# Optimization experiments

Hardware: AMD Instinct MI355X
Metric: run time of the kernel (lower is better)

The kernel has to match this reference:

```python
import jax, jax.numpy as jnp
import numpy as np

B, T, HID = 2, 2048, 1024
NH = 8
QK_DIM = 1024
V_DIM = 2048
SCALE_BASE = 512.0
GN_EPS = 1e-5


def _xpos_rotate(x, downscale):
    # x: [B, T, QK_DIM]; XPOS rotary embedding (syncdoth/RetNet, offset=0)
    d = QK_DIM
    dh = d // 2
    pos = jnp.arange(T, dtype=jnp.float32)
    # per-pair magnitude scale
    base_scale = (jnp.arange(0, d, 2, dtype=jnp.float32) + 0.4 * d) / (1.4 * d)  # [dh]
    scale = base_scale[None, :] ** (pos[:, None] / SCALE_BASE)  # [T, dh]
    if downscale:
        scale = 1.0 / scale
    inv_freq = 1.0 / (10000.0 ** (jnp.arange(dh, dtype=jnp.float32) / dh))
    sinusoid = pos[:, None] * inv_freq[None, :]  # [T, dh]
    sin = jnp.sin(sinusoid) * scale
    cos = jnp.cos(sinusoid) * scale
    # duplicate_interleave -> [T, d]
    sin = jnp.repeat(sin, 2, axis=-1)
    cos = jnp.repeat(cos, 2, axis=-1)
    x1 = x[..., 0::2]
    x2 = x[..., 1::2]
    rot = jnp.stack((-x2, x1), axis=-1).reshape(x.shape)  # rotate_every_two
    return x * cos[None] + rot * sin[None]


def setup_inputs() -> dict:
    key = jax.random.key(0)
    k1, k2, k3, k4 = jax.random.split(key, 4)
    x = jax.random.normal(k1, (B, T, HID), dtype=jnp.float32)
    Wqkv = jax.random.normal(k2, (HID, 2 * QK_DIM + V_DIM), dtype=jnp.float32) / np.sqrt(HID)
    Wg = jax.random.normal(k3, (HID, V_DIM), dtype=jnp.float32) / np.sqrt(HID)
    Wp = jax.random.normal(k4, (V_DIM, HID), dtype=jnp.float32) / np.sqrt(V_DIM)
    bp = jnp.zeros((HID,), dtype=jnp.float32)
    return {"x": x, "Wqkv": Wqkv, "Wg": Wg, "Wp": Wp, "bp": bp}


def reference(x, Wqkv, Wg, Wp, bp):
    # multi-scale decay (non-default gamma path)
    gamma = 1.0 - jnp.exp(jnp.linspace(np.log(1.0 / 32), np.log(1.0 / 512), NH)).astype(jnp.float32)  # [NH]

    qkv = x @ Wqkv  # [B,T,2qk+v]
    q, k, v = jnp.split(qkv, [QK_DIM, 2 * QK_DIM], axis=-1)
    q = _xpos_rotate(q, downscale=False)
    k = _xpos_rotate(k, downscale=True)

    dqk = QK_DIM // NH
    dv = V_DIM // NH
    q = q.reshape(B, T, NH, dqk).transpose(0, 2, 1, 3)  # [B,H,T,dqk]
    k = k.reshape(B, T, NH, dqk).transpose(0, 2, 1, 3)
    v = v.reshape(B, T, NH, dv).transpose(0, 2, 1, 3)   # [B,H,T,dv]

    # parallel decay mask: gamma^(i-j) for i>=j else 0  -> [H,T,T]
    idx = jnp.arange(T)
    expo = idx[:, None] - idx[None, :]
    expo_safe = jnp.where(expo >= 0, expo, 0).astype(jnp.float32)
    decay_mask = jnp.where(expo[None] >= 0, gamma[:, None, None] ** expo_safe[None], 0.0)  # [H,T,T]

    scores = jnp.einsum('bhid,bhjd->bhij', q, k) * (dqk ** -0.5)
    retention = jnp.einsum('bhij,bhjv->bhiv', scores * decay_mask[None], v)  # [B,H,T,dv]

    # current_kv state: sum_t decay_mask[h,-1,t] * k_t (outer) v_t  -> [B,H,dqk,dv]
    curr_kv = jnp.einsum('bhtk,bhtv,ht->bhkv', k, v, decay_mask[:, -1, :])

    ret = retention.transpose(0, 2, 1, 3).reshape(B, T, V_DIM)

    # GroupNorm(num_groups=NH, affine=False) over [B*T, V_DIM]
    g = ret.reshape(B, T, NH, dv)
    mu = jnp.mean(g, axis=-1, keepdims=True)
    var = jnp.var(g, axis=-1, keepdims=True)
    normed = ((g - mu) / jnp.sqrt(var + GN_EPS)).reshape(B, T, V_DIM)

    gate = jax.nn.silu(x @ Wg)
    out = (gate * normed) @ Wp + bp
    return out, curr_kv
```

## Files before the change

### kernel.cpp

```cpp
#include <hip/hip_runtime.h>

typedef unsigned short u16;
typedef unsigned int   u32;
typedef unsigned long long u64;

typedef __attribute__((ext_vector_type(8))) short bf8_t;
typedef __attribute__((ext_vector_type(4))) float f4_t;

#define DEVI __device__ __forceinline__
#define MFMA16(a,b,c) __builtin_amdgcn_mfma_f32_16x16x32_bf16((a),(b),(c),0,0,0)

#define BB   2
#define TT   2048
#define HIDN 1024
#define L0f  (-3.4657359027997265f)
#define DLf  (-0.3960841031714215f)
#define SCL  (0.08838834764831845f)

DEVI u16 f2b(float f) {
    u32 u = __float_as_uint(f);
    u += 0x7FFFu + ((u >> 16) & 1u);
    return (u16)(u >> 16);
}
DEVI float b2f(u16 u) { return __uint_as_float(((u32)u) << 16); }

DEVI void gll16(const void* g, void* l) {
    __builtin_amdgcn_global_load_lds((const __attribute__((address_space(1))) void*)g,
                                     (__attribute__((address_space(3))) void*)l, 16, 0, 0);
}

__global__ __launch_bounds__(256) void k_prep(
    const float* __restrict__ x, const float* __restrict__ Wqkv,
    const float* __restrict__ Wg, const float* __restrict__ Wp,
    u32* __restrict__ cqp, u32* __restrict__ ckp,
    float* __restrict__ gt, float* __restrict__ gk,
    u16* __restrict__ xb, u16* __restrict__ oQ, u16* __restrict__ oG, u16* __restrict__ oP) {
    int bx = blockIdx.x;
    if (bx < 4096) {
        int idx = bx * 256 + threadIdx.x;
        int t = idx >> 9, m = idx & 511;
        float base = (2.f * (float)m + 409.6f) * (1.f / 1433.6f);
        float s = exp2f(log2f(base) * ((float)t * (1.f / 512.f)));
        float invf = exp2f(-(float)m * (13.287712379549449f / 512.f));
        float sn, cs;
        sincosf((float)t * invf, &sn, &cs);
        int h = m >> 6;
        float lg2h = log2f(1.f - expf(L0f + (float)h * DLf));
        float qf = s * SCL * exp2f((float)(t & 63) * lg2h);
        cqp[idx] = (u32)f2b(cs * qf) | ((u32)f2b(sn * qf) << 16);
        float is = 1.f / s;
        ckp[idx] = (u32)f2b(cs * is) | ((u32)f2b(sn * is) << 16);
        return;
    }
    if (bx < 4162) {
        int i = (bx - 4096) * 256 + threadIdx.x;
        if (i < 16384) {
            int h = i >> 11, t = i & 2047;
            float lg2 = log2f(1.f - expf(L0f + (float)h * DLf));
            gt[i] = exp2f((float)(2047 - t) * lg2);
        } else {
            int idx = i - 16384;
            int h = idx >> 6, d = idx & 63;
            float lg2 = log2f(1.f - expf(L0f + (float)h * DLf));
            gk[idx] = exp2f(-(float)d * lg2);
        }
        return;
    }
    if (bx < 12354) {
        __shared__ float tile[32][33];
        int b2 = bx - 4162;
        const float* in; u16* out; int R, C, cx, ry;
        if (b2 < 4096)      { in = Wqkv; out = oQ; R = 1024; C = 4096; cx = b2 & 127; ry = b2 >> 7; }
        else if (b2 < 6144) { int b3 = b2 - 4096; in = Wg; out = oG; R = 1024; C = 2048; cx = b3 & 63; ry = b3 >> 6; }
        else                { int b3 = b2 - 6144; in = Wp; out = oP; R = 2048; C = 1024; cx = b3 & 31; ry = b3 >> 5; }
        int c0 = cx * 32, r0 = ry * 32;
        int tx = threadIdx.x & 31, ty = threadIdx.x >> 5;
#pragma unroll
        for (int i = 0; i < 4; i++)
            tile[ty * 4 + i][tx] = in[(size_t)(r0 + ty * 4 + i) * C + c0 + tx];
        __syncthreads();
#pragma unroll
        for (int i = 0; i < 4; i++)
            out[(size_t)(c0 + ty * 4 + i) * R + r0 + tx] = f2b(tile[tx][ty * 4 + i]);
        return;
    }
    {
        int i = (bx - 12354) * 256 + threadIdx.x;
        float4 v = ((const float4*)x)[i];
        u64 pk = (u64)f2b(v.x) | ((u64)f2b(v.y) << 16) | ((u64)f2b(v.z) << 32) | ((u64)f2b(v.w) << 48);
        ((u64*)xb)[i] = pk;
    }
}

DEVI void stage_chunk(const u16* __restrict__ A, const u16* __restrict__ B,
                      int m0, int n0, int kt, char* buf, int id, int wid, int lane) {
    int j = id & 3;
    int flat = j * 8192 + wid * 1024 + lane * 16;
    int row = flat >> 7, byt = (flat & 127) ^ ((row & 7) << 4);
    if (id < 4)
        gll16((const char*)A + (size_t)(m0 + row) * 2048 + kt * 128 + byt,
              buf + j * 8192 + wid * 1024);
    else
        gll16((const char*)B + (size_t)(n0 + row) * 2048 + kt * 128 + byt,
              buf + 32768 + j * 8192 + wid * 1024);
}

#define QCORE(kk, fmh, LOADB)                                                         \
    {                                                                                 \
        bf8_t a_[4];                                                                  \
        _Pragma("unroll")                                                             \
        for (int f = 0; f < 4; f++) {                                                 \
            int ra = 128 * wr + ((fmh) * 4 + f) * 16 + lr;                            \
            a_[f] = *(const bf8_t*)(bA + ra * 128 + (((kk) * 64 + lg * 16) ^ ((ra & 7) << 4))); \
        }                                                                             \
        if (LOADB) {                                                                  \
            _Pragma("unroll")                                                         \
            for (int f = 0; f < 4; f++) {                                             \
                int rb = 64 * wc + f * 16 + lr;                                       \
                breg[f] = *(const bf8_t*)(bB + rb * 128 + (((kk) * 64 + lg * 16) ^ ((rb & 7) << 4))); \
            }                                                                         \
        }                                                                             \
        __builtin_amdgcn_s_barrier();                                                 \
        __builtin_amdgcn_s_setprio(1);                                                \
        _Pragma("unroll")                                                             \
        for (int f = 0; f < 4; f++)                                                   \
            _Pragma("unroll")                                                         \
            for (int j = 0; j < 4; j++)                                               \
                acc[(fmh) * 4 + f][j] = MFMA16(a_[f], breg[j], acc[(fmh) * 4 + f][j]); \
        __builtin_amdgcn_s_setprio(0);                                                \
    }

__global__ __launch_bounds__(512, 2) void k_gemm_qkvg8(
    const u16* __restrict__ xb, const u16* __restrict__ Wcat,
    const u32* __restrict__ cqp, const u32* __restrict__ ckp, const float* __restrict__ gkt,
    u16* __restrict__ qw, u16* __restrict__ kw, u16* __restrict__ kT, u16* __restrict__ vT,
    u16* __restrict__ gateb) {
    __shared__ __align__(16) char L[131072];
    int flat = blockIdx.x;
    int swz = (flat & 7) * 48 + (flat >> 3);
    int m0 = (swz / 24) * 256, n0 = (swz % 24) * 256;
    int tid = threadIdx.x, lane = tid & 63, wid = tid >> 6;
    int wr = wid >> 2, wc = wid & 3, lr = lane & 15, lg = lane >> 4;
    f4_t acc[8][4];
#pragma unroll
    for (int i = 0; i < 8; i++)
#pragma unroll
        for (int j = 0; j < 4; j++)
#pragma unroll
            for (int e = 0; e < 4; e++) acc[i][j][e] = 0.f;
    stage_chunk(xb, Wcat, m0, n0, 0, L, 0, wid, lane);
    stage_chunk(xb, Wcat, m0, n0, 0, L, 2, wid, lane);
    stage_chunk(xb, Wcat, m0, n0, 0, L, 4, wid, lane);
    stage_chunk(xb, Wcat, m0, n0, 0, L, 5, wid, lane);
    stage_chunk(xb, Wcat, m0, n0, 0, L, 6, wid, lane);
    stage_chunk(xb, Wcat, m0, n0, 0, L, 7, wid, lane);
    stage_chunk(xb, Wcat, m0, n0, 0, L, 1, wid, lane);
    stage_chunk(xb, Wcat, m0, n0, 0, L, 3, wid, lane);
    asm volatile("s_waitcnt vmcnt(2)" ::: "memory");
    __builtin_amdgcn_s_barrier();
    for (int kt = 0; kt < 16; ++kt) {
        const char* bA = L + (kt & 1) * 65536;
        const char* bB = bA + 32768;
        char* nbuf = L + ((kt + 1) & 1) * 65536;
        bf8_t breg[4];
        if (kt < 15) {
            stage_chunk(xb, Wcat, m0, n0, kt + 1, nbuf, 0, wid, lane);
            stage_chunk(xb, Wcat, m0, n0, kt + 1, nbuf, 2, wid, lane);
        }
        QCORE(0, 0, 1)
        if (kt < 15) { asm volatile("s_waitcnt vmcnt(2)" ::: "memory"); }
        else         { asm volatile("s_waitcnt vmcnt(0)" ::: "memory"); }
        __builtin_amdgcn_s_barrier();
        if (kt < 15) {
            stage_chunk(xb, Wcat, m0, n0, kt + 1, nbuf, 4, wid, lane);
            stage_chunk(xb, Wcat, m0, n0, kt + 1, nbuf, 5, wid, lane);
        }
        QCORE(0, 1, 0)
        __builtin_amdgcn_s_barrier();
        if (kt < 15) {
            stage_chunk(xb, Wcat, m0, n0, kt + 1, nbuf, 6, wid, lane);
            stage_chunk(xb, Wcat, m0, n0, kt + 1, nbuf, 7, wid, lane);
        }
        QCORE(1, 0, 1)
        __builtin_amdgcn_s_barrier();
        if (kt < 15) {
            stage_chunk(xb, Wcat, m0, n0, kt + 1, nbuf, 1, wid, lane);
            stage_chunk(xb, Wcat, m0, n0, kt + 1, nbuf, 3, wid, lane);
        }
        QCORE(1, 1, 0)
        if (kt < 15) { asm volatile("s_waitcnt vmcnt(2)" ::: "memory"); }
        __builtin_amdgcn_s_barrier();
    }
    __syncthreads();
    char* SP = L;
    int b = m0 >> 11, t0 = m0 & 2047;
    if (n0 < 4096 && n0 >= 2048) {
        int h = (n0 - 2048) >> 8;
#pragma unroll
        for (int fm = 0; fm < 8; fm++)
#pragma unroll
            for (int fn = 0; fn < 4; fn++) {
                int dv = wc * 64 + fn * 16 + lr;
                int rowb = wr * 128 + fm * 16 + lg * 4;
                u64 pk = 0;
#pragma unroll
                for (int r = 0; r < 4; r++) pk |= ((u64)f2b(acc[fm][fn][r])) << (16 * r);
                *(u64*)(SP + dv * 512 + ((rowb * 2) ^ ((dv & 15) << 4))) = pk;
            }
        __syncthreads();
#pragma unroll
        for (int it = 0; it < 16; it++) {
            int chunk = it * 512 + tid;
            int dv = chunk >> 5, j = chunk & 31;
            uint4 v = *(const uint4*)(SP + dv * 512 + ((j * 16) ^ ((dv & 15) << 4)));
            *(uint4*)(vT + ((size_t)((b * 8 + h) * 256 + dv)) * 2048 + t0 + j * 8) = v;
        }
    } else if (n0 < 2048) {
        int isK = n0 >= 1024;
        const u32* cT = isK ? ckp : cqp;
        int hb = (n0 >> 7) & 7;
#pragma unroll
        for (int fm = 0; fm < 8; fm++)
#pragma unroll
            for (int fn = 0; fn < 4; fn++) {
                int col = wc * 64 + fn * 16 + lr;
                int gq = (n0 & 1023) + col;
                int mi = gq >> 1, h = gq >> 7;
                u64 pk = 0;
#pragma unroll
                for (int r = 0; r < 4; r++) {
                    int rowl = wr * 128 + fm * 16 + lg * 4 + r;
                    int t = t0 + rowl;
                    float v = acc[fm][fn][r];
                    float pv = __shfl_xor(v, 1);
                    u32 cp = cT[t * 512 + mi];
                    float cs = b2f((u16)cp), sn = b2f((u16)(cp >> 16));
                    float o = (col & 1) ? (v * cs + pv * sn) : (v * cs - pv * sn);
                    if (isK) {
                        pk |= ((u64)f2b(o)) << (16 * r);
                        o *= gkt[h * 64 + (t & 63)];
                    }
                    *(u16*)(SP + rowl * 512 + ((col * 2) ^ ((rowl & 15) << 4))) = f2b(o);
                }
                if (isK)
                    *(u64*)&kT[((size_t)((b * 8 + h) * 128 + (gq & 127))) * 2048 + t0 + wr * 128 + fm * 16 + lg * 4] = pk;
            }
        __syncthreads();
#pragma unroll
        for (int it = 0; it < 16; it++) {
            int chunk = it * 512 + tid;
            int r = chunk >> 5, j = chunk & 31;
            uint4 v = *(const uint4*)(SP + r * 512 + ((j * 16) ^ ((r & 15) << 4)));
            int hh = hb + (j >> 4);
            u16* g = (isK ? kw : qw) + ((size_t)((b * 8 + hh) * 2048 + t0 + r)) * 128 + (j & 15) * 8;
            *(uint4*)g = v;
        }
    } else {
        int c0 = n0 - 4096;
#pragma unroll
        for (int fm = 0; fm < 8; fm++)
#pragma unroll
            for (int fn = 0; fn < 4; fn++) {
                int col = wc * 64 + fn * 16 + lr;
#pragma unroll
                for (int r = 0; r < 4; r++) {
                    int rowl = wr * 128 + fm * 16 + lg * 4 + r;
                    float gg = acc[fm][fn][r];
                    *(u16*)(SP + rowl * 512 + ((col * 2) ^ ((rowl & 15) << 4))) = f2b(gg / (1.f + expf(-gg)));
                }
            }
        __syncthreads();
#pragma unroll
        for (int it = 0; it < 16; it++) {
            int chunk = it * 512 + tid;
            int r = chunk >> 5, j = chunk & 31;
            uint4 v = *(const uint4*)(SP + r * 512 + ((j * 16) ^ ((r & 15) << 4)));
            *(uint4*)(gateb + (size_t)(b * 2048 + t0 + r) * 2048 + c0 + j * 8) = v;
        }
    }
}

DEVI void stage_o(const u16* __restrict__ A, const u16* __restrict__ B,
                  int m0, int n0, int kt, char* buf, int id, int wid, int lane) {
    int j = id & 1;
    int flat = j * 8192 + wid * 1024 + lane * 16;
    int row = flat >> 7, byt = (flat & 127) ^ ((row & 7) << 4);
    if (id < 2)
        gll16((const char*)A + (size_t)(m0 + row) * 4096 + kt * 128 + byt,
              buf + j * 8192 + wid * 1024);
    else
        gll16((const char*)B + (size_t)(n0 + row) * 4096 + kt * 128 + byt,
              buf + 16384 + j * 8192 + wid * 1024);
}

__global__ __launch_bounds__(512, 2) void k_gemm_out2(const u16* __restrict__ gdb,
                                                      const u16* __restrict__ Wt,
                                                      const float* __restrict__ bp,
                                                      float* __restrict__ outp) {
    __shared__ __align__(16) char Lo[98304];
    int m0 = blockIdx.y * 128, n0 = blockIdx.x * 128;
    int tid = threadIdx.x, lane = tid & 63, wid = tid >> 6;
    int wr = wid >> 1, wc = wid & 1, lr = lane & 15, lg = lane >> 4;
    f4_t acc[2][4];
#pragma unroll
    for (int i = 0; i < 2; i++)
#pragma unroll
        for (int j = 0; j < 4; j++)
#pragma unroll
            for (int e = 0; e < 4; e++) acc[i][j][e] = 0.f;
#pragma unroll
    for (int c = 0; c < 4; c++) stage_o(gdb, Wt, m0, n0, 0, Lo, c, wid, lane);
#pragma unroll
    for (int c = 0; c < 4; c++) stage_o(gdb, Wt, m0, n0, 1, Lo + 32768, c, wid, lane);
    asm volatile("s_waitcnt vmcnt(4)" ::: "memory");
    __builtin_amdgcn_s_barrier();
    for (int kt = 0; kt < 32; ++kt) {
        const char* bA = Lo + (kt % 3) * 32768;
        const char* bB = bA + 16384;
        if (kt < 30) {
            char* nbuf = Lo + ((kt + 2) % 3) * 32768;
#pragma unroll
            for (int c = 0; c < 4; c++) stage_o(gdb, Wt, m0, n0, kt + 2, nbuf, c, wid, lane);
        }
        __builtin_amdgcn_s_setprio(1);
#pragma unroll
        for (int kk = 0; kk < 2; kk++) {
            bf8_t a[2], b[4];
#pragma unroll
            for (int f = 0; f < 2; f++) {
                int ra = wr * 32 + f * 16 + lr;
                a[f] = *(const bf8_t*)(bA + ra * 128 + ((kk * 64 + lg * 16) ^ ((ra & 7) << 4)));
            }
#pragma unroll
            for (int f = 0; f < 4; f++) {
                int rb = wc * 64 + f * 16 + lr;
                b[f] = *(const bf8_t*)(bB + rb * 128 + ((kk * 64 + lg * 16) ^ ((rb & 7) << 4)));
            }
#pragma unroll
            for (int i = 0; i < 2; i++)
#pragma unroll
                for (int j = 0; j < 4; j++)
                    acc[i][j] = MFMA16(a[i], b[j], acc[i][j]);
        }
        __builtin_amdgcn_s_setprio(0);
        if (kt < 30) { asm volatile("s_waitcnt vmcnt(4)" ::: "memory"); }
        else         { asm volatile("s_waitcnt vmcnt(0)" ::: "memory"); }
        __builtin_amdgcn_s_barrier();
    }
    __syncthreads();
    float* SMf = (float*)Lo;
    float bv[4];
#pragma unroll
    for (int fn = 0; fn < 4; fn++) bv[fn] = bp[n0 + wc * 64 + fn * 16 + lr];
#pragma unroll
    for (int fm = 0; fm < 2; fm++)
#pragma unroll
        for (int fn = 0; fn < 4; fn++) {
            int col = wc * 64 + fn * 16 + lr;
#pragma unroll
            for (int r = 0; r < 4; r++) {
                int rowl = wr * 32 + fm * 16 + lg * 4 + r;
                *(float*)((char*)SMf + rowl * 512 + ((col * 4) ^ ((rowl & 7) << 6))) = acc[fm][fn][r] + bv[fn];
            }
        }
    __syncthreads();
#pragma unroll
    for (int it2 = 0; it2 < 8; it2++) {
        int chunk = it2 * 512 + tid;
        int rowl = chunk >> 5, j = chunk & 31;
        f4_t v = *(const f4_t*)((const char*)SMf + rowl * 512 + ((j * 16) ^ ((rowl & 7) << 6)));
        *(f4_t*)((char*)outp + ((size_t)(m0 + rowl) * 1024 + n0) * 4 + j * 16) = v;
    }
}

DEVI void acc_zero(f4_t acc[4][4]) {
#pragma unroll
    for (int i = 0; i < 4; i++)
#pragma unroll
        for (int j = 0; j < 4; j++)
#pragma unroll
            for (int e = 0; e < 4; e++) acc[i][j][e] = 0.f;
}

__global__ __launch_bounds__(256, 3) void k_retention(const u16* __restrict__ qws, const u16* __restrict__ kws,
                                                      const u16* __restrict__ vTws,
                                                      u16* __restrict__ ret0, u16* __restrict__ ret1) {
    __shared__ u16 SMr[64 * 128 + 256 * 64];
    u16* Ks = SMr;
    u16* Vs = SMr + 64 * 128;
    int x = blockIdx.x;
    int it, jlo, jhi, toret1;
    if (x < 16)      { it = 15 - x;  jlo = 0;              jhi = it + 1;         toret1 = 0; }
    else if (x < 32) { it = x;       jlo = 0;              jhi = (it + 2) >> 1;  toret1 = 0; }
    else             { it = x - 16;  jlo = (it + 2) >> 1;  jhi = it + 1;         toret1 = 1; }
    int h = blockIdx.y, b = blockIdx.z;
    int bh = b * 8 + h;
    float lg2 = log2f(1.f - expf(L0f + (float)h * DLf));
    int i0 = it * 64;
    const u16* qbase = qws + (size_t)bh * 2048 * 128;
    const u16* kbase = kws + (size_t)bh * 2048 * 128;
    const u16* vbase = vTws + (size_t)bh * 256 * 2048;
    int tid = threadIdx.x, lane = tid & 63, w = tid >> 6, lr = lane & 15, lg = lane >> 4;
    bf8_t aq[4];
#pragma unroll
    for (int kk = 0; kk < 4; kk++)
        aq[kk] = *(const bf8_t*)((const char*)qbase + (size_t)(i0 + w * 16 + lr) * 256 + kk * 64 + lg * 16);
    f4_t racc[16];
#pragma unroll
    for (int f = 0; f < 16; f++)
#pragma unroll
        for (int e = 0; e < 4; e++) racc[f][e] = 0.f;
    for (int jt = jlo; jt < jhi; jt++) {
        int j0 = jt * 64;
        int diag = (jt == it);
        float tf = exp2f(64.f * (float)(it - jt) * lg2);
        __syncthreads();
#pragma unroll
        for (int p = 0; p < 4; p++) {
            int flat = p * 4096 + tid * 16;
            int row = flat >> 8, byt = (flat & 255) ^ ((row & 7) << 4);
            gll16((const char*)kbase + (size_t)(j0 + row) * 256 + byt, (char*)Ks + p * 4096 + w * 1024);
        }
#pragma unroll
        for (int p = 0; p < 8; p++) {
            int flat = p * 4096 + tid * 16;
            int row = flat >> 7, byt = (flat & 127) ^ ((row & 7) << 4);
            gll16((const char*)vbase + (size_t)row * 4096 + (size_t)j0 * 2 + byt,
                  (char*)Vs + p * 4096 + w * 1024);
        }
        __syncthreads();
        f4_t sacc[4];
#pragma unroll
        for (int f = 0; f < 4; f++)
#pragma unroll
            for (int e = 0; e < 4; e++) sacc[f][e] = 0.f;
#pragma unroll
        for (int kk = 0; kk < 4; kk++)
#pragma unroll
            for (int fn = 0; fn < 4; fn++) {
                int rb = fn * 16 + lr;
                bf8_t bb = *(const bf8_t*)((const char*)Ks + rb * 256 + ((kk * 64 + lg * 16) ^ ((rb & 7) << 4)));
                sacc[fn] = MFMA16(aq[kk], bb, sacc[fn]);
            }
        __syncthreads();
#pragma unroll
        for (int fn = 0; fn < 4; fn++)
#pragma unroll
            for (int r = 0; r < 4; r++) {
                int i_loc = w * 16 + lg * 4 + r;
                int col = fn * 16 + lr;
                float v = diag ? ((i_loc - col >= 0) ? sacc[fn][r] : 0.f) : sacc[fn][r] * tf;
                *(u16*)((char*)Ks + i_loc * 128 + ((col * 2) ^ ((i_loc & 7) << 4))) = f2b(v);
            }
#pragma unroll
        for (int kk = 0; kk < 2; kk++) {
            int ra = w * 16 + lr;
            bf8_t ap = *(const bf8_t*)((const char*)Ks + ra * 128 + ((kk * 64 + lg * 16) ^ ((ra & 7) << 4)));
#pragma unroll
            for (int fn2 = 0; fn2 < 16; fn2++) {
                int rb = fn2 * 16 + lr;
                bf8_t bv = *(const bf8_t*)((const char*)Vs + rb * 128 + ((kk * 64 + lg * 16) ^ ((rb & 7) << 4)));
                racc[fn2] = MFMA16(ap, bv, racc[fn2]);
            }
        }
    }
    __syncthreads();
    u16* St = Vs;
#pragma unroll
    for (int fn2 = 0; fn2 < 16; fn2++)
#pragma unroll
        for (int r = 0; r < 4; r++) {
            int il = w * 16 + lg * 4 + r;
            int dv = fn2 * 16 + lr;
            *(u16*)((char*)St + il * 512 + ((dv * 2) ^ ((il & 15) << 4))) = f2b(racc[fn2][r]);
        }
    __syncthreads();
#pragma unroll
    for (int it2 = 0; it2 < 8; it2++) {
        int chunk = it2 * 256 + tid;
        int il = chunk >> 5, j = chunk & 31;
        uint4 v = *(const uint4*)((const char*)St + il * 512 + ((j * 16) ^ ((il & 15) << 4)));
        char* dst;
        if (toret1) dst = (char*)ret1 + ((size_t)(b * 1024 + i0 - 1024 + il) * 2048 + h * 256) * 2 + j * 16;
        else        dst = (char*)ret0 + ((size_t)(b * 2048 + i0 + il) * 2048 + h * 256) * 2 + j * 16;
        *(uint4*)dst = v;
    }
}

__global__ __launch_bounds__(512) void k_currkv(const u16* __restrict__ kTws, const u16* __restrict__ vTws,
                                                const float* __restrict__ gtab, float* __restrict__ part) {
    __shared__ u16 Ks2[128 * 64];
    __shared__ u16 Vws[256 * 64];
    int tr = blockIdx.x;
    int bh = blockIdx.y;
    int h = bh & 7;
    const u16* kT = kTws + (size_t)bh * 128 * 2048;
    const u16* vT = vTws + (size_t)bh * 256 * 2048;
    const float* gt = gtab + h * 2048;
    int tid = threadIdx.x, lane = tid & 63, wid = tid >> 6;
    int wr = wid >> 2, wc = wid & 3, lr = lane & 15, lg = lane >> 4;
    f4_t acc[4][4]; acc_zero(acc);
    for (int tc = 0; tc < 4; tc++) {
        int t0 = tr * 256 + tc * 64;
        __syncthreads();
#pragma unroll
        for (int p = 0; p < 2; p++) {
            int flat = p * 8192 + tid * 16;
            int row = flat >> 7, byt = (flat & 127) ^ ((row & 7) << 4);
            gll16((const char*)kT + (size_t)row * 4096 + (size_t)t0 * 2 + byt,
                  (char*)Ks2 + p * 8192 + wid * 1024);
        }
#pragma unroll
        for (int p = 0; p < 4; p++) {
            int flat = p * 8192 + tid * 16;
            int row = flat >> 7, byt = flat & 127;
            int tt = t0 + (byt >> 1);
            const u16* src = vT + (size_t)row * 2048 + tt;
            u16 tmp[8]; *(uint4*)tmp = *(const uint4*)src;
            const float* gp = gt + tt;
            u16 op[8];
#pragma unroll
            for (int e = 0; e < 8; e++) op[e] = f2b(b2f(tmp[e]) * gp[e]);
            *(uint4*)((char*)Vws + row * 128 + (byt ^ ((row & 7) << 4))) = *(uint4*)op;
        }
        __syncthreads();
#pragma unroll
        for (int kk = 0; kk < 2; kk++) {
            bf8_t a[4], bb[4];
#pragma unroll
            for (int f = 0; f < 4; f++) {
                int ra = wr * 64 + f * 16 + lr;
                a[f] = *(const bf8_t*)((const char*)Ks2 + ra * 128 + ((kk * 64 + lg * 16) ^ ((ra & 7) << 4)));
                int rb = wc * 64 + f * 16 + lr;
                bb[f] = *(const bf8_t*)((const char*)Vws + rb * 128 + ((kk * 64 + lg * 16) ^ ((rb & 7) << 4)));
            }
#pragma unroll
            for (int i = 0; i < 4; i++)
#pragma unroll
                for (int j = 0; j < 4; j++)
                    acc[i][j] = MFMA16(a[i], bb[j], acc[i][j]);
        }
    }
#pragma unroll
    for (int fm = 0; fm < 4; fm++)
#pragma unroll
        for (int fn = 0; fn < 4; fn++)
#pragma unroll
            for (int r = 0; r < 4; r++) {
                int dk = wr * 64 + fm * 16 + lg * 4 + r;
                int dv = wc * 64 + fn * 16 + lr;
                part[((size_t)(bh * 8 + tr)) * 32768 + (size_t)dk * 256 + dv] = acc[fm][fn][r];
            }
}

__global__ __launch_bounds__(256) void k_reduce_ckv(const float* __restrict__ part, float* __restrict__ outc) {
    int i = blockIdx.x * 256 + threadIdx.x;
    int bh = i >> 15, wv = i & 32767;
    float s = 0.f;
#pragma unroll
    for (int tr = 0; tr < 8; tr++) s += part[((size_t)(bh * 8 + tr)) * 32768 + wv];
    outc[i] = s;
}

__global__ __launch_bounds__(256) void k_gnorm(const u16* __restrict__ ret0, const u16* __restrict__ ret1,
                                               const u16* __restrict__ gateb, u16* __restrict__ gatedb) {
    int wv = threadIdx.x >> 6, lane = threadIdx.x & 63;
    int g = blockIdx.x * 8 + wv * 2 + (lane >> 5);
    int l32 = lane & 31;
    int row = g >> 3, h = g & 7;
    size_t base = (size_t)row * 2048 + h * 256 + l32 * 8;
    uint4 p0 = *(const uint4*)(ret0 + base);
    float e[8];
    e[0] = b2f((u16)p0.x); e[1] = b2f((u16)(p0.x >> 16));
    e[2] = b2f((u16)p0.y); e[3] = b2f((u16)(p0.y >> 16));
    e[4] = b2f((u16)p0.z); e[5] = b2f((u16)(p0.z >> 16));
    e[6] = b2f((u16)p0.w); e[7] = b2f((u16)(p0.w >> 16));
    if ((row & 2047) >= 1024) {
        size_t b1 = (size_t)((row >> 11) * 1024 + (row & 1023)) * 2048 + h * 256 + l32 * 8;
        uint4 p1 = *(const uint4*)(ret1 + b1);
        e[0] += b2f((u16)p1.x); e[1] += b2f((u16)(p1.x >> 16));
        e[2] += b2f((u16)p1.y); e[3] += b2f((u16)(p1.y >> 16));
        e[4] += b2f((u16)p1.z); e[5] += b2f((u16)(p1.z >> 16));
        e[6] += b2f((u16)p1.w); e[7] += b2f((u16)(p1.w >> 16));
    }
    float s = 0.f, sqs = 0.f;
#pragma unroll
    for (int i = 0; i < 8; i++) { s += e[i]; sqs += e[i] * e[i]; }
#pragma unroll
    for (int m = 1; m < 32; m <<= 1) { s += __shfl_xor(s, m); sqs += __shfl_xor(sqs, m); }
    float mean = s * (1.f / 256.f);
    float var = sqs * (1.f / 256.f) - mean * mean;
    float inv = rsqrtf(var + 1e-5f);
    uint4 gp = *(const uint4*)(gateb + base);
    u32 gw[4] = {gp.x, gp.y, gp.z, gp.w};
    uint4 ov;
    u32* op = (u32*)&ov;
#pragma unroll
    for (int i = 0; i < 4; i++) {
        float g0 = b2f((u16)gw[i]), g1 = b2f((u16)(gw[i] >> 16));
        op[i] = (u32)f2b((e[2 * i] - mean) * inv * g0) |
                ((u32)f2b((e[2 * i + 1] - mean) * inv * g1) << 16);
    }
    *(uint4*)(gatedb + base) = ov;
}

extern "C" void kernel_launch(void* const* d_in, const int* in_sizes, int n_in,
                              void* d_out, int out_size, void* d_ws, size_t ws_size,
                              hipStream_t stream) {
    const float* x    = (const float*)d_in[0];
    const float* Wqkv = (const float*)d_in[1];
    const float* Wg   = (const float*)d_in[2];
    const float* Wp   = (const float*)d_in[3];
    const float* bp   = (const float*)d_in[4];
    float* outp   = (float*)d_out;
    float* outckv = outp + (size_t)BB * TT * HIDN;

    char* ws = (char*)d_ws;
    const size_t MB = 1024 * 1024;
    u16*   xb     = (u16*)(ws);
    u16*   WqkvT  = (u16*)(ws + 8 * MB);
    u16*   WgT    = (u16*)(ws + 16 * MB);
    u16*   WpT    = (u16*)(ws + 20 * MB);
    u32*   cqp    = (u32*)(ws + 24 * MB);
    u32*   ckp    = (u32*)(ws + 28 * MB);
    u16*   gateb  = (u16*)(ws + 32 * MB);
    u16*   qw     = (u16*)(ws + 48 * MB);
    u16*   kw     = (u16*)(ws + 56 * MB);
    u16*   kT     = (u16*)(ws + 64 * MB);
    u16*   vT     = (u16*)(ws + 72 * MB);
    u16*   ret0b  = (u16*)(ws + 88 * MB);
    u16*   ret1b  = (u16*)(ws + 104 * MB);
    float* ckvp   = (float*)(ws + 88 * MB);
    float* gtab   = (float*)(ws + 120 * MB);
    float* gkt    = (float*)(ws + 120 * MB + 65536);
    u16*   gatedb = (u16*)(ws + 48 * MB);

    hipLaunchKernelGGL(k_prep, dim3(16450), dim3(256), 0, stream,
                       x, Wqkv, Wg, Wp, cqp, ckp, gtab, gkt, xb, WqkvT, WgT, WpT);
    hipLaunchKernelGGL(k_gemm_qkvg8, dim3(384), dim3(512), 0, stream,
                       xb, WqkvT, cqp, ckp, gkt, qw, kw, kT, vT, gateb);
    hipLaunchKernelGGL(k_currkv, dim3(8, 16), dim3(512), 0, stream, kT, vT, gtab, ckvp);
    hipLaunchKernelGGL(k_reduce_ckv, dim3(2048), dim3(256), 0, stream, ckvp, outckv);
    hipLaunchKernelGGL(k_retention, dim3(48, 8, 2), dim3(256), 0, stream, qw, kw, vT, ret0b, ret1b);
    hipLaunchKernelGGL(k_gnorm, dim3(4096), dim3(256), 0, stream, ret0b, ret1b, gateb, gatedb);
    hipLaunchKernelGGL(k_gemm_out2, dim3(8, 32), dim3(512), 0, stream, gatedb, WpT, bp, outp);
}
```

Before: 204.8 us.

## Double-buffer V tiles in retention and drop split-row scheduling

The retention kernel no longer splits long rows across two blocks with a separate ret1 buffer. Each block now handles a full row tile with a 1D grid of 512 blocks, pairing short and long rows in the ordering to balance load. V tiles are double-buffered in shared memory, with the next tile's async loads overlapping the current MFMA work via explicit vmcnt waits and raw barriers. This removes the ret1 add in the group-norm kernel, but doubles LDS use, lowers occupancy to 2 blocks per CU, and relies on hand-placed wait counts for correctness.

```diff
diff --git a/kernel.cpp b/kernel.cpp
--- a/kernel.cpp
+++ b/kernel.cpp
@@ -382,21 +382,19 @@
             for (int e = 0; e < 4; e++) acc[i][j][e] = 0.f;
 }
 
-__global__ __launch_bounds__(256, 3) void k_retention(const u16* __restrict__ qws, const u16* __restrict__ kws,
-                                                      const u16* __restrict__ vTws,
-                                                      u16* __restrict__ ret0, u16* __restrict__ ret1) {
-    __shared__ u16 SMr[64 * 128 + 256 * 64];
+__global__ __launch_bounds__(256, 2) void k_retention(const u16* __restrict__ qws, const u16* __restrict__ kws,
+                                                      const u16* __restrict__ vTws, u16* __restrict__ ret) {
+    __shared__ u16 SMr[64 * 128 + 2 * 256 * 64];
     u16* Ks = SMr;
-    u16* Vs = SMr + 64 * 128;
-    int x = blockIdx.x;
-    int it, jlo, jhi, toret1;
-    if (x < 16)      { it = 15 - x;  jlo = 0;              jhi = it + 1;         toret1 = 0; }
-    else if (x < 32) { it = x;       jlo = 0;              jhi = (it + 2) >> 1;  toret1 = 0; }
-    else             { it = x - 16;  jlo = (it + 2) >> 1;  jhi = it + 1;         toret1 = 1; }
-    int h = blockIdx.y, b = blockIdx.z;
-    int bh = b * 8 + h;
+    u16* Vs0 = SMr + 64 * 128;
+    int Lb = blockIdx.x;
+    int half = Lb >> 8, sub = Lb & 255;
+    int itt = sub & 31;
+    int it = half ? 31 - itt : itt;
+    int bh = (sub >> 5) + half * 8;
+    int b = bh >> 3, h = bh & 7;
     float lg2 = log2f(1.f - expf(L0f + (float)h * DLf));
-    int i0 = it * 64;
+    int i0 = it * 64, nj = it + 1;
     const u16* qbase = qws + (size_t)bh * 2048 * 128;
     const u16* kbase = kws + (size_t)bh * 2048 * 128;
     const u16* vbase = vTws + (size_t)bh * 256 * 2048;
@@ -410,25 +408,37 @@
     for (int f = 0; f < 16; f++)
 #pragma unroll
         for (int e = 0; e < 4; e++) racc[f][e] = 0.f;
-    for (int jt = jlo; jt < jhi; jt++) {
+#pragma unroll
+    for (int p = 0; p < 8; p++) {
+        int flat = p * 4096 + tid * 16;
+        int row = flat >> 7, byt = (flat & 127) ^ ((row & 7) << 4);
+        gll16((const char*)vbase + (size_t)row * 4096 + byt, (char*)Vs0 + p * 4096 + w * 1024);
+    }
+    for (int jt = 0; jt < nj; jt++) {
         int j0 = jt * 64;
         int diag = (jt == it);
         float tf = exp2f(64.f * (float)(it - jt) * lg2);
-        __syncthreads();
 #pragma unroll
         for (int p = 0; p < 4; p++) {
             int flat = p * 4096 + tid * 16;
             int row = flat >> 8, byt = (flat & 255) ^ ((row & 7) << 4);
             gll16((const char*)kbase + (size_t)(j0 + row) * 256 + byt, (char*)Ks + p * 4096 + w * 1024);
         }
-#pragma unroll
-        for (int p = 0; p < 8; p++) {
-            int flat = p * 4096 + tid * 16;
-            int row = flat >> 7, byt = (flat & 127) ^ ((row & 7) << 4);
-            gll16((const char*)vbase + (size_t)row * 4096 + (size_t)j0 * 2 + byt,
-                  (char*)Vs + p * 4096 + w * 1024);
-        }
-        __syncthreads();
+        if (jt + 1 < nj) {
+            char* Vn = (char*)Vs0 + ((jt + 1) & 1) * 32768;
+#pragma unroll
+            for (int p = 0; p < 8; p++) {
+                int flat = p * 4096 + tid * 16;
+                int row = flat >> 7, byt = (flat & 127) ^ ((row & 7) << 4);
+                gll16((const char*)vbase + (size_t)row * 4096 + (size_t)(j0 + 64) * 2 + byt,
+                      Vn + p * 4096 + w * 1024);
+            }
+            asm volatile("s_waitcnt vmcnt(8)" ::: "memory");
+        } else {
+            asm volatile("s_waitcnt vmcnt(0)" ::: "memory");
+        }
+        __builtin_amdgcn_s_barrier();
+        const char* Vc = (const char*)Vs0 + (jt & 1) * 32768;
         f4_t sacc[4];
 #pragma unroll
         for (int f = 0; f < 4; f++)
@@ -442,7 +452,7 @@
                 bf8_t bb = *(const bf8_t*)((const char*)Ks + rb * 256 + ((kk * 64 + lg * 16) ^ ((rb & 7) << 4)));
                 sacc[fn] = MFMA16(aq[kk], bb, sacc[fn]);
             }
-        __syncthreads();
+        __builtin_amdgcn_s_barrier();
 #pragma unroll
         for (int fn = 0; fn < 4; fn++)
 #pragma unroll
@@ -459,13 +469,14 @@
 #pragma unroll
             for (int fn2 = 0; fn2 < 16; fn2++) {
                 int rb = fn2 * 16 + lr;
-                bf8_t bv = *(const bf8_t*)((const char*)Vs + rb * 128 + ((kk * 64 + lg * 16) ^ ((rb & 7) << 4)));
+                bf8_t bv = *(const bf8_t*)(Vc + rb * 128 + ((kk * 64 + lg * 16) ^ ((rb & 7) << 4)));
                 racc[fn2] = MFMA16(ap, bv, racc[fn2]);
             }
         }
+        __builtin_amdgcn_s_barrier();
     }
     __syncthreads();
-    u16* St = Vs;
+    u16* St = Vs0;
 #pragma unroll
     for (int fn2 = 0; fn2 < 16; fn2++)
 #pragma unroll
@@ -480,10 +491,7 @@
         int chunk = it2 * 256 + tid;
         int il = chunk >> 5, j = chunk & 31;
         uint4 v = *(const uint4*)((const char*)St + il * 512 + ((j * 16) ^ ((il & 15) << 4)));
-        char* dst;
-        if (toret1) dst = (char*)ret1 + ((size_t)(b * 1024 + i0 - 1024 + il) * 2048 + h * 256) * 2 + j * 16;
-        else        dst = (char*)ret0 + ((size_t)(b * 2048 + i0 + il) * 2048 + h * 256) * 2 + j * 16;
-        *(uint4*)dst = v;
+        *(uint4*)((char*)ret + ((size_t)(b * 2048 + i0 + il) * 2048 + h * 256) * 2 + j * 16) = v;
     }
 }
 
@@ -562,27 +570,19 @@
     outc[i] = s;
 }
 
-__global__ __launch_bounds__(256) void k_gnorm(const u16* __restrict__ ret0, const u16* __restrict__ ret1,
-                                               const u16* __restrict__ gateb, u16* __restrict__ gatedb) {
+__global__ __launch_bounds__(256) void k_gnorm(const u16* __restrict__ ret, const u16* __restrict__ gateb,
+                                               u16* __restrict__ gatedb) {
     int wv = threadIdx.x >> 6, lane = threadIdx.x & 63;
     int g = blockIdx.x * 8 + wv * 2 + (lane >> 5);
     int l32 = lane & 31;
     int row = g >> 3, h = g & 7;
     size_t base = (size_t)row * 2048 + h * 256 + l32 * 8;
-    uint4 p0 = *(const uint4*)(ret0 + base);
+    uint4 p0 = *(const uint4*)(ret + base);
     float e[8];
     e[0] = b2f((u16)p0.x); e[1] = b2f((u16)(p0.x >> 16));
     e[2] = b2f((u16)p0.y); e[3] = b2f((u16)(p0.y >> 16));
     e[4] = b2f((u16)p0.z); e[5] = b2f((u16)(p0.z >> 16));
     e[6] = b2f((u16)p0.w); e[7] = b2f((u16)(p0.w >> 16));
-    if ((row & 2047) >= 1024) {
-        size_t b1 = (size_t)((row >> 11) * 1024 + (row & 1023)) * 2048 + h * 256 + l32 * 8;
-        uint4 p1 = *(const uint4*)(ret1 + b1);
-        e[0] += b2f((u16)p1.x); e[1] += b2f((u16)(p1.x >> 16));
-        e[2] += b2f((u16)p1.y); e[3] += b2f((u16)(p1.y >> 16));
-        e[4] += b2f((u16)p1.z); e[5] += b2f((u16)(p1.z >> 16));
-        e[6] += b2f((u16)p1.w); e[7] += b2f((u16)(p1.w >> 16));
-    }
     float s = 0.f, sqs = 0.f;
 #pragma unroll
     for (int i = 0; i < 8; i++) { s += e[i]; sqs += e[i] * e[i]; }
@@ -628,8 +628,7 @@
     u16*   kw     = (u16*)(ws + 56 * MB);
     u16*   kT     = (u16*)(ws + 64 * MB);
     u16*   vT     = (u16*)(ws + 72 * MB);
-    u16*   ret0b  = (u16*)(ws + 88 * MB);
-    u16*   ret1b  = (u16*)(ws + 104 * MB);
+    u16*   retb   = (u16*)(ws + 88 * MB);
     float* ckvp   = (float*)(ws + 88 * MB);
     float* gtab   = (float*)(ws + 120 * MB);
     float* gkt    = (float*)(ws + 120 * MB + 65536);
@@ -641,7 +640,7 @@
                        xb, WqkvT, cqp, ckp, gkt, qw, kw, kT, vT, gateb);
     hipLaunchKernelGGL(k_currkv, dim3(8, 16), dim3(512), 0, stream, kT, vT, gtab, ckvp);
     hipLaunchKernelGGL(k_reduce_ckv, dim3(2048), dim3(256), 0, stream, ckvp, outckv);
-    hipLaunchKernelGGL(k_retention, dim3(48, 8, 2), dim3(256), 0, stream, qw, kw, vT, ret0b, ret1b);
-    hipLaunchKernelGGL(k_gnorm, dim3(4096), dim3(256), 0, stream, ret0b, ret1b, gateb, gatedb);
+    hipLaunchKernelGGL(k_retention, dim3(512), dim3(256), 0, stream, qw, kw, vT, retb);
+    hipLaunchKernelGGL(k_gnorm, dim3(4096), dim3(256), 0, stream, retb, gateb, gatedb);
     hipLaunchKernelGGL(k_gemm_out2, dim3(8, 32), dim3(512), 0, stream, gatedb, WpT, bp, outp);
 }
```

New measurement: 211.7 us. +3.4%, slower.
